# Kernel optimization log

Measured on AMD Instinct MI355X. Metric: run time of the kernel, lower is better.

The kernel has to match this reference:

```python
import jax, jax.numpy as jnp
import numpy as np

# Vim-S config
B, L, D, DEPTH = 16, 197, 384, 24
DI, DS, DTR = 768, 16, 24  # d_inner=2*D, d_state, dt_rank=ceil(D/16)
NUM_CLASSES = 1000
EPS = 1e-5


def setup_inputs() -> dict:
    key = jax.random.key(0)
    ks = jax.random.split(key, 12)
    f = jnp.float32
    rn = lambda k, shp, s=0.02: jax.random.normal(k, shp, f) * s
    inp = {
        'x': jax.random.normal(ks[0], (B, 3, 224, 224), f),
        'patch_w': rn(ks[1], (D, 3, 16, 16)),
        'patch_b': jnp.zeros((D,), f),
        'cls_token': rn(ks[2], (1, 1, D)),
        'pos_embed': rn(ks[3], (1, L, D)),
        'in_proj_w': rn(ks[4], (DEPTH, 2 * DI, D)),
        'conv_w': rn(ks[5], (DEPTH, DI, 1, 4), 0.1),  # depthwise causal conv, d_conv=4
        'conv_b': jnp.zeros((DEPTH, DI), f),
        'x_proj_w': rn(ks[6], (DEPTH, DTR + 2 * DS, DI)),
        'dt_proj_w': rn(ks[7], (DEPTH, DI, DTR), 0.1),
        'dt_proj_b': jnp.full((DEPTH, DI), float(np.log(np.expm1(0.01))), f),
        'A_log': jnp.log(jnp.broadcast_to(jnp.arange(1, DS + 1, dtype=f), (DEPTH, DI, DS))),
        'D_ssm': jnp.ones((DEPTH, DI), f),
        'out_proj_w': rn(ks[8], (DEPTH, D, DI)),
        'norm_w': jnp.ones((DEPTH, D), f),
        'norm_b': jnp.zeros((DEPTH, D), f),
        'normf_w': jnp.ones((D,), f),
        'normf_b': jnp.zeros((D,), f),
        'head_w': rn(ks[9], (NUM_CLASSES, D)),
        'head_b': jnp.zeros((NUM_CLASSES,), f),
    }
    return inp


def _ln(u, w, b):
    mu = u.mean(-1, keepdims=True)
    v = ((u - mu) ** 2).mean(-1, keepdims=True)
    return (u - mu) * jax.lax.rsqrt(v + EPS) * w + b


def _silu(u):
    return u * jax.nn.sigmoid(u)


def _mixer(u, Win, Wc, bc, Wx, Wdt, bdt, Alog, Dp, Wout):
    # u: [B, L, D]
    xz = jnp.einsum('bld,ed->ble', u, Win)            # [B, L, 2*DI]
    xc, z = jnp.split(xz, 2, axis=-1)
    # causal depthwise conv1d (d_conv=4): pad 3 on the left
    xt = jnp.pad(xc.transpose(0, 2, 1), ((0, 0), (0, 0), (3, 0)))
    xt = jax.lax.conv_general_dilated(xt, Wc, (1,), 'VALID',
                                      dimension_numbers=('NCH', 'OIH', 'NCH'),
                                      feature_group_count=DI)
    xc = _silu((xt + bc[None, :, None]).transpose(0, 2, 1))  # [B, L, DI]
    dbl = jnp.einsum('bld,ed->ble', xc, Wx)           # [B, L, DTR+2*DS]
    dt = jax.nn.softplus(jnp.einsum('blr,dr->bld', dbl[..., :DTR], Wdt) + bdt)
    Bm = dbl[..., DTR:DTR + DS]                       # [B, L, DS]
    Cm = dbl[..., DTR + DS:]                          # [B, L, DS]
    A = -jnp.exp(Alog)                                # [DI, DS]
    dA = jnp.exp(jnp.einsum('bld,dn->bldn', dt, A))   # [B, L, DI, DS]
    dBx = jnp.einsum('bld,bln->bldn', dt * xc, Bm)    # [B, L, DI, DS]

    def step(h, inps):
        dA_t, dBx_t, C_t = inps
        h = dA_t * h + dBx_t                          # [B, DI, DS]
        return h, jnp.einsum('bdn,bn->bd', h, C_t)

    h0 = jnp.zeros((u.shape[0], DI, DS), u.dtype)
    _, ys = jax.lax.scan(step, h0, (dA.transpose(1, 0, 2, 3),
                                    dBx.transpose(1, 0, 2, 3),
                                    Cm.transpose(1, 0, 2)))
    y = ys.transpose(1, 0, 2) + xc * Dp               # [B, L, DI]
    y = y * _silu(z)
    return jnp.einsum('ble,de->bld', y, Wout)         # [B, L, D]


def reference(x, patch_w, patch_b, cls_token, pos_embed, in_proj_w, conv_w, conv_b,
              x_proj_w, dt_proj_w, dt_proj_b, A_log, D_ssm, out_proj_w,
              norm_w, norm_b, normf_w, normf_b, head_w, head_b):
    b = x.shape[0]
    # patch embed: Conv2d(3, D, 16, stride 16)
    feat = jax.lax.conv_general_dilated(x, patch_w, (16, 16), 'VALID',
                                        dimension_numbers=('NCHW', 'OIHW', 'NCHW'))
    feat = feat + patch_b[None, :, None, None]
    tokens = feat.reshape(b, D, -1).transpose(0, 2, 1)          # [B, 196, D]
    h = jnp.concatenate([jnp.broadcast_to(cls_token, (b, 1, D)), tokens], axis=1)
    h = h + pos_embed                                           # [B, 197, D]

    def layer(carry, p):
        hid, res = carry
        Win, Wc, bc, Wx, Wdt, bdt, Alog, Dp, Wout, nw, nb = p
        res = res + hid                # (hidden + residual), first layer: residual = hidden
        hid = _mixer(_ln(res, nw, nb), Win, Wc, bc, Wx, Wdt, bdt, Alog, Dp, Wout)
        return (hid, res), None

    (hid, res), _ = jax.lax.scan(layer, (h, jnp.zeros_like(h)),
                                 (in_proj_w, conv_w, conv_b, x_proj_w, dt_proj_w,
                                  dt_proj_b, A_log, D_ssm, out_proj_w, norm_w, norm_b))
    out = _ln(res + hid, normf_w, normf_b)
    return out[:, 0] @ head_w.T + head_b                        # [B, num_classes]
```

## Files before the change

kernel.cpp:

```cpp
#include <hip/hip_runtime.h>
#include <hip/hip_bf16.h>
#include <math.h>

#define BB     16
#define LL     197
#define DD     384
#define DEPTH  24
#define DI     768
#define DSN    16
#define DTR    24
#define NC     1000
#define TT     (BB*LL)
#define NPATCH 196
#define EPSV   1e-5f

#define NCHUNK 12
#define CH     17

typedef __attribute__((ext_vector_type(8))) short short8;
typedef __attribute__((ext_vector_type(4))) short short4v;
typedef __attribute__((ext_vector_type(4))) float f32x4;

__device__ __forceinline__ short f2bf(float f) {
  union { float f; unsigned u; } v; v.f = f;
  unsigned u = v.u + 0x7fffu + ((v.u >> 16) & 1u);
  return (short)(u >> 16);
}

__device__ __forceinline__ void gload16(const short* g, const short* l) {
  __builtin_amdgcn_global_load_lds(
      (const __attribute__((address_space(1))) unsigned int*)g,
      (__attribute__((address_space(3))) unsigned int*)l, 16, 0, 0);
}

__global__ __launch_bounds__(256) void k_cvt4(const float* __restrict__ s0, short* __restrict__ d0, int n0,
                                              const float* __restrict__ s1, short* __restrict__ d1, int n1,
                                              const float* __restrict__ s2, short* __restrict__ d2, int n2,
                                              const float* __restrict__ s3, short* __restrict__ d3, int n3,
                                              int b0, int b1, int b2) {
  int blk = blockIdx.x;
  const float* src; short* dst; int n; int lb;
  if (blk < b0)      { src = s0; dst = d0; n = n0; lb = blk; }
  else if (blk < b1) { src = s1; dst = d1; n = n1; lb = blk - b0; }
  else if (blk < b2) { src = s2; dst = d2; n = n2; lb = blk - b1; }
  else               { src = s3; dst = d3; n = n3; lb = blk - b2; }
  int i = (lb * 256 + threadIdx.x) * 4;
  if (i + 3 < n) {
    float4 v = *(const float4*)&src[i];
    short4v o = {f2bf(v.x), f2bf(v.y), f2bf(v.z), f2bf(v.w)};
    *(short4v*)&dst[i] = o;
  } else {
    for (int j = 0; i + j < n && j < 4; j++) dst[i + j] = f2bf(src[i + j]);
  }
}

__global__ __launch_bounds__(256) void k_init(const float* __restrict__ cls,
                                              const float* __restrict__ pos,
                                              float* __restrict__ res) {
  int i = blockIdx.x * 256 + threadIdx.x;
  if (i < BB * DD) {
    int b = i / DD, d = i % DD;
    res[(size_t)(b * LL) * DD + d] = cls[d] + pos[d];
  }
}

__global__ __launch_bounds__(256) void k_patch(const float* __restrict__ x,
                                               const float* __restrict__ pw,
                                               const float* __restrict__ pb,
                                               const float* __restrict__ pos,
                                               float* __restrict__ res) {
  __shared__ short sA[64 * 40];
  __shared__ short sB[64 * 40];
  const int tid = threadIdx.x;
  const int m0 = blockIdx.x * 64, n0 = blockIdx.y * 64;
  const int srow = tid >> 2;
  const int skq = (tid & 3) * 8;
  const int lane = tid & 63, w = tid >> 6;
  const int wm = (w >> 1) * 32, wn = (w & 1) * 32;
  const int fr = lane & 15;
  const int fk = (lane >> 4) * 8;
  f32x4 acc[2][2] = {};
  const int m = m0 + srow;
  const int b = m / NPATCH;
  const int p = m % NPATCH;
  const int ph = p / 14, pwi = p % 14;
  const float* Wrow = pw + (size_t)(n0 + srow) * 768 + skq;
  for (int k0 = 0; k0 < 768; k0 += 32) {
    int k = k0 + skq;
    int c = k >> 8, rr = (k >> 4) & 15, kw = k & 15;
    const float* xrow = &x[(size_t)(((b * 3 + c) * 224) + (ph * 16 + rr)) * 224 +
                           (pwi * 16 + kw)];
    float4 a0 = *(const float4*)&xrow[0];
    float4 a1 = *(const float4*)&xrow[4];
    float4 b0 = *(const float4*)&Wrow[k0];
    float4 b1 = *(const float4*)&Wrow[k0 + 4];
    short8 av = {f2bf(a0.x), f2bf(a0.y), f2bf(a0.z), f2bf(a0.w),
                 f2bf(a1.x), f2bf(a1.y), f2bf(a1.z), f2bf(a1.w)};
    short8 bv = {f2bf(b0.x), f2bf(b0.y), f2bf(b0.z), f2bf(b0.w),
                 f2bf(b1.x), f2bf(b1.y), f2bf(b1.z), f2bf(b1.w)};
    *(short8*)&sA[srow * 40 + skq] = av;
    *(short8*)&sB[srow * 40 + skq] = bv;
    __syncthreads();
    short8 af0 = *(const short8*)&sA[(wm + fr) * 40 + fk];
    short8 af1 = *(const short8*)&sA[(wm + 16 + fr) * 40 + fk];
    short8 bf0 = *(const short8*)&sB[(wn + fr) * 40 + fk];
    short8 bf1 = *(const short8*)&sB[(wn + 16 + fr) * 40 + fk];
    acc[0][0] = __builtin_amdgcn_mfma_f32_16x16x32_bf16(af0, bf0, acc[0][0], 0, 0, 0);
    acc[0][1] = __builtin_amdgcn_mfma_f32_16x16x32_bf16(af0, bf1, acc[0][1], 0, 0, 0);
    acc[1][0] = __builtin_amdgcn_mfma_f32_16x16x32_bf16(af1, bf0, acc[1][0], 0, 0, 0);
    acc[1][1] = __builtin_amdgcn_mfma_f32_16x16x32_bf16(af1, bf1, acc[1][1], 0, 0, 0);
    __syncthreads();
  }
#pragma unroll
  for (int i = 0; i < 2; i++)
#pragma unroll
    for (int j = 0; j < 2; j++)
#pragma unroll
      for (int q = 0; q < 4; q++) {
        int mm = m0 + wm + i * 16 + (lane >> 4) * 4 + q;
        int nn = n0 + wn + j * 16 + (lane & 15);
        int b2 = mm / NPATCH, pp = mm % NPATCH;
        int tok = b2 * LL + 1 + pp;
        res[(size_t)tok * DD + nn] = acc[i][j][q] + pb[nn] + pos[(size_t)(1 + pp) * DD + nn];
      }
}

__global__ __launch_bounds__(256) void k_gemm128(const short* __restrict__ A, int lda,
                                                 const short* __restrict__ W, int ldb,
                                                 float* __restrict__ C, int ldc,
                                                 int M, int N, int K) {
  __shared__ short sA[128 * 32];
  __shared__ short sB[128 * 32];
  const int tid = threadIdx.x;
  const int lane = tid & 63, w = tid >> 6;
  const int m0 = blockIdx.x * 128, n0 = blockIdx.y * 128;
  const int wm = (w >> 1) * 64, wn = (w & 1) * 64;
  const int fr = lane & 15;
  const int fk = (lane >> 4) * 8;
  const int q0 = w * 2, q1 = w * 2 + 1;
  const int sr0 = q0 * 16 + (lane >> 2);
  const int sr1 = q1 * 16 + (lane >> 2);
  const int scol = (lane & 3) * 8;
  f32x4 acc[4][4] = {};
  const short* Ab0 = A + (size_t)(m0 + sr0) * lda + scol;
  const short* Ab1 = A + (size_t)(m0 + sr1) * lda + scol;
  const short* Bb0 = W + (size_t)(n0 + sr0) * ldb + scol;
  const short* Bb1 = W + (size_t)(n0 + sr1) * ldb + scol;
  for (int k0 = 0; k0 < K; k0 += 32) {
    gload16(Ab0 + k0, &sA[q0 * 512]);
    gload16(Ab1 + k0, &sA[q1 * 512]);
    gload16(Bb0 + k0, &sB[q0 * 512]);
    gload16(Bb1 + k0, &sB[q1 * 512]);
    __syncthreads();
    short8 af[4], bf[4];
#pragma unroll
    for (int i = 0; i < 4; i++) {
      af[i] = *(const short8*)&sA[(wm + i * 16 + fr) * 32 + fk];
      bf[i] = *(const short8*)&sB[(wn + i * 16 + fr) * 32 + fk];
    }
#pragma unroll
    for (int i = 0; i < 4; i++)
#pragma unroll
      for (int j = 0; j < 4; j++)
        acc[i][j] = __builtin_amdgcn_mfma_f32_16x16x32_bf16(af[i], bf[j], acc[i][j], 0, 0, 0);
    __syncthreads();
  }
#pragma unroll
  for (int i = 0; i < 4; i++)
#pragma unroll
    for (int j = 0; j < 4; j++)
#pragma unroll
      for (int q = 0; q < 4; q++) {
        int mm = m0 + wm + i * 16 + (lane >> 4) * 4 + q;
        int nn = n0 + wn + j * 16 + fr;
        if (mm < M) C[(size_t)mm * ldc + nn] = acc[i][j][q];
      }
}

__global__ __launch_bounds__(256) void k_gemm64(const short* __restrict__ A, int lda,
                                                const short* __restrict__ W, int ldb,
                                                float* __restrict__ C, int ldc,
                                                int M, int N, int K) {
  __shared__ short sA[64 * 32];
  __shared__ short sB[64 * 32];
  const int tid = threadIdx.x;
  const int lane = tid & 63, w = tid >> 6;
  const int m0 = blockIdx.x * 64, n0 = blockIdx.y * 64;
  const int wm = (w >> 1) * 32, wn = (w & 1) * 32;
  const int fr = lane & 15;
  const int fk = (lane >> 4) * 8;
  const int srow = w * 16 + (lane >> 2);
  const int scol = (lane & 3) * 8;
  f32x4 acc[2][2] = {};
  const short* Ab = A + (size_t)(m0 + srow) * lda + scol;
  const short* Bb = W + (size_t)(n0 + srow) * ldb + scol;
  for (int k0 = 0; k0 < K; k0 += 32) {
    gload16(Ab + k0, &sA[w * 512]);
    gload16(Bb + k0, &sB[w * 512]);
    __syncthreads();
    short8 af0 = *(const short8*)&sA[(wm + fr) * 32 + fk];
    short8 af1 = *(const short8*)&sA[(wm + 16 + fr) * 32 + fk];
    short8 bf0 = *(const short8*)&sB[(wn + fr) * 32 + fk];
    short8 bf1 = *(const short8*)&sB[(wn + 16 + fr) * 32 + fk];
    acc[0][0] = __builtin_amdgcn_mfma_f32_16x16x32_bf16(af0, bf0, acc[0][0], 0, 0, 0);
    acc[0][1] = __builtin_amdgcn_mfma_f32_16x16x32_bf16(af0, bf1, acc[0][1], 0, 0, 0);
    acc[1][0] = __builtin_amdgcn_mfma_f32_16x16x32_bf16(af1, bf0, acc[1][0], 0, 0, 0);
    acc[1][1] = __builtin_amdgcn_mfma_f32_16x16x32_bf16(af1, bf1, acc[1][1], 0, 0, 0);
    __syncthreads();
  }
#pragma unroll
  for (int i = 0; i < 2; i++)
#pragma unroll
    for (int j = 0; j < 2; j++)
#pragma unroll
      for (int q = 0; q < 4; q++) {
        int mm = m0 + wm + i * 16 + (lane >> 4) * 4 + q;
        int nn = n0 + wn + j * 16 + fr;
        if (mm < M) C[(size_t)mm * ldc + nn] += acc[i][j][q];
      }
}

__global__ __launch_bounds__(256) void k_conv(const float* __restrict__ xz,
                                              const float* __restrict__ wc,
                                              const float* __restrict__ bc,
                                              float* __restrict__ xc,
                                              short* __restrict__ xcbf) {
  int i = blockIdx.x * 256 + threadIdx.x;
  if (i >= TT * (DI / 4)) return;
  int eg = i % (DI / 4);
  int t = i / (DI / 4);
  int e = eg * 4;
  int b = t / LL, l = t % LL;
  const float* base = xz + (size_t)(b * LL) * (2 * DI) + e;
  float4 w0 = *(const float4*)&wc[(e + 0) * 4];
  float4 w1 = *(const float4*)&wc[(e + 1) * 4];
  float4 w2 = *(const float4*)&wc[(e + 2) * 4];
  float4 w3 = *(const float4*)&wc[(e + 3) * 4];
  float4 acc = *(const float4*)&bc[e];
  if (l >= 3) {
    float4 xv = *(const float4*)&base[(size_t)(l - 3) * (2 * DI)];
    acc.x += xv.x * w0.x; acc.y += xv.y * w1.x; acc.z += xv.z * w2.x; acc.w += xv.w * w3.x;
  }
  if (l >= 2) {
    float4 xv = *(const float4*)&base[(size_t)(l - 2) * (2 * DI)];
    acc.x += xv.x * w0.y; acc.y += xv.y * w1.y; acc.z += xv.z * w2.y; acc.w += xv.w * w3.y;
  }
  if (l >= 1) {
    float4 xv = *(const float4*)&base[(size_t)(l - 1) * (2 * DI)];
    acc.x += xv.x * w0.z; acc.y += xv.y * w1.z; acc.z += xv.z * w2.z; acc.w += xv.w * w3.z;
  }
  {
    float4 xv = *(const float4*)&base[(size_t)l * (2 * DI)];
    acc.x += xv.x * w0.w; acc.y += xv.y * w1.w; acc.z += xv.z * w2.w; acc.w += xv.w * w3.w;
  }
  acc.x = acc.x / (1.f + __expf(-acc.x));
  acc.y = acc.y / (1.f + __expf(-acc.y));
  acc.z = acc.z / (1.f + __expf(-acc.z));
  acc.w = acc.w / (1.f + __expf(-acc.w));
  *(float4*)&xc[(size_t)t * DI + e] = acc;
  short4v ov = {f2bf(acc.x), f2bf(acc.y), f2bf(acc.z), f2bf(acc.w)};
  *(short4v*)&xcbf[(size_t)t * DI + e] = ov;
}

__global__ __launch_bounds__(256, 1) void k_xd(const short* __restrict__ xcbf,
                                               const short* __restrict__ wx,
                                               const short* __restrict__ wdt,
                                               const float* __restrict__ dbias,
                                               float* __restrict__ dbl,
                                               float* __restrict__ dtb) {
  __shared__ short sDT[16 * 40];
  const int tid = threadIdx.x;
  const int t0 = blockIdx.x * 16;
  const int lane = tid & 63, w = tid >> 6;
  const int fr = lane & 15;
  const int fk = (lane >> 4) * 8;
  f32x4 acc0 = {}, acc1 = {};
  const short* Arow = xcbf + (size_t)(t0 + fr) * DI + fk;
  const short* Wrow = wx + (size_t)(w * 16 + fr) * DI + fk;
#pragma unroll
  for (int k0 = 0; k0 < DI; k0 += 64) {
    short8 af0 = *(const short8*)&Arow[k0];
    short8 bf0 = *(const short8*)&Wrow[k0];
    short8 af1 = *(const short8*)&Arow[k0 + 32];
    short8 bf1 = *(const short8*)&Wrow[k0 + 32];
    acc0 = __builtin_amdgcn_mfma_f32_16x16x32_bf16(af0, bf0, acc0, 0, 0, 0);
    acc1 = __builtin_amdgcn_mfma_f32_16x16x32_bf16(af1, bf1, acc1, 0, 0, 0);
  }
  f32x4 accx = acc0 + acc1;
  {
    int nn = w * 16 + fr;
#pragma unroll
    for (int q = 0; q < 4; q++) {
      int row = (lane >> 4) * 4 + q;
      int t = t0 + row;
      if (nn >= DTR && nn < 56) dbl[(size_t)t * 56 + nn] = accx[q];
      if (w < 2) sDT[row * 40 + nn] = (nn < DTR) ? f2bf(accx[q]) : (short)0;
    }
  }
  __syncthreads();
  short8 adt = *(const short8*)&sDT[fr * 40 + fk];
  const int g = lane >> 4;
#pragma unroll
  for (int jj = 0; jj < 12; jj++) {
    int j = w * 12 + jj;
    short8 bdt = short8{0, 0, 0, 0, 0, 0, 0, 0};
    if (g < 3) bdt = *(const short8*)&wdt[(size_t)(j * 16 + fr) * DTR + g * 8];
    f32x4 p = {};
    p = __builtin_amdgcn_mfma_f32_16x16x32_bf16(adt, bdt, p, 0, 0, 0);
    int nc = j * 16 + fr;
    float bv = dbias[nc];
#pragma unroll
    for (int q = 0; q < 4; q++) {
      int t = t0 + (lane >> 4) * 4 + q;
      float v = p[q] + bv;
      v = (v > 20.f) ? v : __logf(1.f + __expf(v));
      dtb[(size_t)t * DI + nc] = v;
    }
  }
}

__global__ __launch_bounds__(256) void k_scan1(const float* __restrict__ dt,
                                               const float* __restrict__ xc,
                                               const float* __restrict__ dbl,
                                               const float* __restrict__ Alog,
                                               float* __restrict__ Aprod,
                                               float* __restrict__ Hend) {
  const int tid = threadIdx.x;
  const int e = blockIdx.x * 128 + (tid >> 1);
  const int nh = tid & 1;
  const int b = blockIdx.y;
  const int c = blockIdx.z;
  float4 al0 = *(const float4*)&Alog[(size_t)e * DSN + nh * 8];
  float4 al1 = *(const float4*)&Alog[(size_t)e * DSN + nh * 8 + 4];
  float negA[8] = {-__expf(al0.x), -__expf(al0.y), -__expf(al0.z), -__expf(al0.w),
                   -__expf(al1.x), -__expf(al1.y), -__expf(al1.z), -__expf(al1.w)};
  float h[8] = {};
  float asum = 0.f;
  const int l0 = c * CH;
  const int l1 = (l0 + CH < LL) ? (l0 + CH) : LL;
  const size_t tbase = (size_t)b * LL;
  for (int l = l0; l < l1; l++) {
    size_t t = tbase + l;
    float dtv = dt[t * DI + e];
    float xcv = xc[t * DI + e];
    float4 B0 = *(const float4*)&dbl[t * 56 + DTR + nh * 8];
    float4 B1 = *(const float4*)&dbl[t * 56 + DTR + nh * 8 + 4];
    float dx = dtv * xcv;
    float Bv[8] = {B0.x, B0.y, B0.z, B0.w, B1.x, B1.y, B1.z, B1.w};
#pragma unroll
    for (int j = 0; j < 8; j++)
      h[j] = __expf(dtv * negA[j]) * h[j] + dx * Bv[j];
    asum += dtv;
  }
  size_t ci = (((size_t)c * BB + b) * DI + e) * DSN + nh * 8;
  *(float4*)&Aprod[ci] = float4{__expf(asum * negA[0]), __expf(asum * negA[1]),
                                __expf(asum * negA[2]), __expf(asum * negA[3])};
  *(float4*)&Aprod[ci + 4] = float4{__expf(asum * negA[4]), __expf(asum * negA[5]),
                                    __expf(asum * negA[6]), __expf(asum * negA[7])};
  *(float4*)&Hend[ci] = float4{h[0], h[1], h[2], h[3]};
  *(float4*)&Hend[ci + 4] = float4{h[4], h[5], h[6], h[7]};
}

__global__ __launch_bounds__(256) void k_scan2(const float* __restrict__ dt,
                                               const float* __restrict__ xc,
                                               const float* __restrict__ xz,
                                               const float* __restrict__ dbl,
                                               const float* __restrict__ Alog,
                                               const float* __restrict__ Dp,
                                               const float* __restrict__ Aprod,
                                               const float* __restrict__ Hend,
                                               short* __restrict__ ybf) {
  const int tid = threadIdx.x;
  const int e = blockIdx.x * 128 + (tid >> 1);
  const int nh = tid & 1;
  const int b = blockIdx.y;
  const int c = blockIdx.z;
  float4 al0 = *(const float4*)&Alog[(size_t)e * DSN + nh * 8];
  float4 al1 = *(const float4*)&Alog[(size_t)e * DSN + nh * 8 + 4];
  float negA[8] = {-__expf(al0.x), -__expf(al0.y), -__expf(al0.z), -__expf(al0.w),
                   -__expf(al1.x), -__expf(al1.y), -__expf(al1.z), -__expf(al1.w)};
  const float dpv = Dp[e];
  float h[8] = {};
  const size_t cstride = (size_t)BB * DI * DSN;
  const size_t cbase = (((size_t)b * DI + e) * DSN) + nh * 8;
  for (int cp = 0; cp < c; cp++) {
    size_t ci = (size_t)cp * cstride + cbase;
    float4 a0 = *(const float4*)&Aprod[ci];
    float4 a1 = *(const float4*)&Aprod[ci + 4];
    float4 e0 = *(const float4*)&Hend[ci];
    float4 e1 = *(const float4*)&Hend[ci + 4];
    h[0] = a0.x * h[0] + e0.x; h[1] = a0.y * h[1] + e0.y;
    h[2] = a0.z * h[2] + e0.z; h[3] = a0.w * h[3] + e0.w;
    h[4] = a1.x * h[4] + e1.x; h[5] = a1.y * h[5] + e1.y;
    h[6] = a1.z * h[6] + e1.z; h[7] = a1.w * h[7] + e1.w;
  }
  const int l0 = c * CH;
  const int l1 = (l0 + CH < LL) ? (l0 + CH) : LL;
  const size_t tbase = (size_t)b * LL;
  for (int l = l0; l < l1; l++) {
    size_t t = tbase + l;
    float dtv = dt[t * DI + e];
    float xcv = xc[t * DI + e];
    float zv = xz[t * (2 * DI) + DI + e];
    float4 B0 = *(const float4*)&dbl[t * 56 + DTR + nh * 8];
    float4 B1 = *(const float4*)&dbl[t * 56 + DTR + nh * 8 + 4];
    float4 C0 = *(const float4*)&dbl[t * 56 + DTR + DSN + nh * 8];
    float4 C1 = *(const float4*)&dbl[t * 56 + DTR + DSN + nh * 8 + 4];
    float dx = dtv * xcv;
    float Bv[8] = {B0.x, B0.y, B0.z, B0.w, B1.x, B1.y, B1.z, B1.w};
    float Cv[8] = {C0.x, C0.y, C0.z, C0.w, C1.x, C1.y, C1.z, C1.w};
    float acc = 0.f;
#pragma unroll
    for (int j = 0; j < 8; j++) {
      h[j] = __expf(dtv * negA[j]) * h[j] + dx * Bv[j];
      acc += h[j] * Cv[j];
    }
    acc += __shfl_xor(acc, 1);
    if (nh == 0) {
      float sz = zv * (1.f / (1.f + __expf(-zv)));
      ybf[t * DI + e] = f2bf((acc + xcv * dpv) * sz);
    }
  }
}

__global__ __launch_bounds__(256) void k_ln(const float* __restrict__ res,
                                            short* __restrict__ u,
                                            const float* __restrict__ nw,
                                            const float* __restrict__ nb) {
  const int lane = threadIdx.x & 63;
  const int t = blockIdx.x * 4 + (threadIdx.x >> 6);
  float r[6];
  float s = 0.f, sq = 0.f;
#pragma unroll
  for (int j = 0; j < 6; j++) {
    int d = lane + j * 64;
    float v = res[(size_t)t * DD + d];
    r[j] = v;
    s += v; sq += v * v;
  }
#pragma unroll
  for (int o = 32; o > 0; o >>= 1) { s += __shfl_xor(s, o); sq += __shfl_xor(sq, o); }
  float mu = s * (1.f / 384.f);
  float var = sq * (1.f / 384.f) - mu * mu;
  float rs = rsqrtf(var + EPSV);
#pragma unroll
  for (int j = 0; j < 6; j++) {
    int d = lane + j * 64;
    u[(size_t)t * DD + d] = f2bf((r[j] - mu) * rs * nw[d] + nb[d]);
  }
}

__global__ __launch_bounds__(256) void k_final(const float* __restrict__ res,
                                               const float* __restrict__ nfw,
                                               const float* __restrict__ nfb,
                                               const float* __restrict__ hw,
                                               const float* __restrict__ hb,
                                               float* __restrict__ out) {
  const int b = blockIdx.y;
  const int c0 = blockIdx.x * 125;
  const int tid = threadIdx.x;
  __shared__ float u0[DD];
  __shared__ float ls[4], lq[4];
  const size_t t0 = (size_t)b * LL * DD;
  float v0 = res[t0 + tid];
  float v1 = (tid < 128) ? res[t0 + 256 + tid] : 0.f;
  float s = v0 + v1, sq = v0 * v0 + v1 * v1;
#pragma unroll
  for (int o = 32; o > 0; o >>= 1) { s += __shfl_xor(s, o); sq += __shfl_xor(sq, o); }
  if ((tid & 63) == 0) { ls[tid >> 6] = s; lq[tid >> 6] = sq; }
  __syncthreads();
  float st = ls[0] + ls[1] + ls[2] + ls[3];
  float qt = lq[0] + lq[1] + lq[2] + lq[3];
  float mu = st * (1.f / 384.f);
  float var = qt * (1.f / 384.f) - mu * mu;
  float rs = rsqrtf(var + EPSV);
  u0[tid] = (v0 - mu) * rs * nfw[tid] + nfb[tid];
  if (tid < 128) u0[256 + tid] = (v1 - mu) * rs * nfw[256 + tid] + nfb[256 + tid];
  __syncthreads();
  int c = c0 + tid;
  if (tid < 125 && c < NC) {
    float acc = hb[c];
    const float* wrow = hw + (size_t)c * DD;
    for (int d = 0; d < DD; d += 4) {
      float4 w4 = *(const float4*)&wrow[d];
      acc += u0[d] * w4.x + u0[d + 1] * w4.y + u0[d + 2] * w4.z + u0[d + 3] * w4.w;
    }
    out[(size_t)b * NC + c] = acc;
  }
}

extern "C" void kernel_launch(void* const* d_in, const int* in_sizes, int n_in,
                              void* d_out, int out_size, void* d_ws, size_t ws_size,
                              hipStream_t stream) {
  const float* x       = (const float*)d_in[0];
  const float* patch_w = (const float*)d_in[1];
  const float* patch_b = (const float*)d_in[2];
  const float* cls     = (const float*)d_in[3];
  const float* pos     = (const float*)d_in[4];
  const float* in_proj = (const float*)d_in[5];
  const float* conv_w  = (const float*)d_in[6];
  const float* conv_b  = (const float*)d_in[7];
  const float* x_proj  = (const float*)d_in[8];
  const float* dt_w    = (const float*)d_in[9];
  const float* dt_b    = (const float*)d_in[10];
  const float* A_log   = (const float*)d_in[11];
  const float* D_ssm   = (const float*)d_in[12];
  const float* out_w   = (const float*)d_in[13];
  const float* norm_w  = (const float*)d_in[14];
  const float* norm_b  = (const float*)d_in[15];
  const float* normf_w = (const float*)d_in[16];
  const float* normf_b = (const float*)d_in[17];
  const float* head_w  = (const float*)d_in[18];
  const float* head_b  = (const float*)d_in[19];
  float* out = (float*)d_out;

  float* ws = (float*)d_ws;
  float* res = ws;  ws += (size_t)TT * DD;
  float* u_r = ws;  ws += (size_t)TT * DD;
  float* xzb = ws;  ws += (size_t)TT * 2 * DI;
  float* xcb = ws;  ws += (size_t)TT * DI;
  float* dbl = ws;  ws += (size_t)TT * 56;
  float* dtb = ws;  ws += (size_t)TT * DI;
  float* ybf_r = ws; ws += (size_t)TT * DI / 2;
  float* xcbf_r = ws; ws += (size_t)TT * DI / 2;
  float* Aprod = ws; ws += (size_t)NCHUNK * BB * DI * DSN;
  float* Hend  = ws; ws += (size_t)NCHUNK * BB * DI * DSN;
  short* winbf  = (short*)ws; ws += (size_t)DEPTH * 2 * DI * DD / 2;
  short* woutbf = (short*)ws; ws += (size_t)DEPTH * DD * DI / 2;
  short* wxbf   = (short*)ws; ws += (size_t)DEPTH * 56 * DI / 2;
  short* wdtbf  = (short*)ws; ws += (size_t)DEPTH * DI * DTR / 2;

  short* u    = (short*)u_r;
  short* ybf  = (short*)ybf_r;
  short* xcbf = (short*)xcbf_r;

  {
    int n1 = DEPTH * 2 * DI * DD;
    int n2 = DEPTH * DD * DI;
    int n3 = DEPTH * 56 * DI;
    int n4 = DEPTH * DI * DTR;
    int g1 = (n1 / 4 + 255) / 256;
    int g2 = (n2 / 4 + 255) / 256;
    int g3 = (n3 / 4 + 255) / 256;
    int g4 = (n4 / 4 + 255) / 256;
    k_cvt4<<<g1 + g2 + g3 + g4, 256, 0, stream>>>(
        in_proj, winbf, n1, out_w, woutbf, n2, x_proj, wxbf, n3, dt_w, wdtbf, n4,
        g1, g1 + g2, g1 + g2 + g3);
  }

  k_init<<<(BB * DD + 255) / 256, 256, 0, stream>>>(cls, pos, res);
  k_patch<<<dim3(49, 6), 256, 0, stream>>>(x, patch_w, patch_b, pos, res);

  for (int layer = 0; layer < DEPTH; layer++) {
    k_ln<<<TT / 4, 256, 0, stream>>>(res, u, norm_w + layer * DD,
                                     norm_b + layer * DD);
    k_gemm128<<<dim3(25, 12), 256, 0, stream>>>(
        u, DD, winbf + (size_t)layer * 2 * DI * DD, DD, xzb, 2 * DI, TT, 2 * DI, DD);
    k_conv<<<(TT * (DI / 4) + 255) / 256, 256, 0, stream>>>(
        xzb, conv_w + layer * DI * 4, conv_b + layer * DI, xcb, xcbf);
    k_xd<<<dim3(TT / 16), 256, 0, stream>>>(
        xcbf, wxbf + (size_t)layer * 56 * DI, wdtbf + (size_t)layer * DI * DTR,
        dt_b + layer * DI, dbl, dtb);
    k_scan1<<<dim3(DI / 128, BB, NCHUNK - 1), 256, 0, stream>>>(
        dtb, xcb, dbl, A_log + (size_t)layer * DI * DSN, Aprod, Hend);
    k_scan2<<<dim3(DI / 128, BB, NCHUNK), 256, 0, stream>>>(
        dtb, xcb, xzb, dbl, A_log + (size_t)layer * DI * DSN,
        D_ssm + layer * DI, Aprod, Hend, ybf);
    k_gemm64<<<dim3(50, 6), 256, 0, stream>>>(
        ybf, DI, woutbf + (size_t)layer * DD * DI, DI, res, DD, TT, DD, DI);
  }

  k_final<<<dim3(8, BB), 256, 0, stream>>>(res, normf_w, normf_b, head_w, head_b, out);
}
```

Before: 2.632 ms.

## Fuse two-pass chunked selective scan into one kernel with LDS carry exchange

```diff
diff --git a/kernel.cpp b/kernel.cpp
--- a/kernel.cpp
+++ b/kernel.cpp
@@ -319,84 +319,57 @@
   }
 }
 
-__global__ __launch_bounds__(256) void k_scan1(const float* __restrict__ dt,
-                                               const float* __restrict__ xc,
-                                               const float* __restrict__ dbl,
-                                               const float* __restrict__ Alog,
-                                               float* __restrict__ Aprod,
-                                               float* __restrict__ Hend) {
+__global__ __launch_bounds__(768) void k_scan(const float* __restrict__ dt,
+                                              const float* __restrict__ xc,
+                                              const float* __restrict__ xz,
+                                              const float* __restrict__ dbl,
+                                              const float* __restrict__ Alog,
+                                              const float* __restrict__ Dp,
+                                              short* __restrict__ ybf) {
+  __shared__ float carry[NCHUNK][32][2][17];
   const int tid = threadIdx.x;
-  const int e = blockIdx.x * 128 + (tid >> 1);
-  const int nh = tid & 1;
-  const int b = blockIdx.y;
-  const int c = blockIdx.z;
+  const int c  = tid >> 6;
+  const int nh = (tid >> 5) & 1;
+  const int el = tid & 31;
+  const int e  = blockIdx.x * 32 + el;
+  const int b  = blockIdx.y;
   float4 al0 = *(const float4*)&Alog[(size_t)e * DSN + nh * 8];
   float4 al1 = *(const float4*)&Alog[(size_t)e * DSN + nh * 8 + 4];
   float negA[8] = {-__expf(al0.x), -__expf(al0.y), -__expf(al0.z), -__expf(al0.w),
                    -__expf(al1.x), -__expf(al1.y), -__expf(al1.z), -__expf(al1.w)};
-  float h[8] = {};
-  float asum = 0.f;
   const int l0 = c * CH;
   const int l1 = (l0 + CH < LL) ? (l0 + CH) : LL;
   const size_t tbase = (size_t)b * LL;
-  for (int l = l0; l < l1; l++) {
-    size_t t = tbase + l;
-    float dtv = dt[t * DI + e];
-    float xcv = xc[t * DI + e];
-    float4 B0 = *(const float4*)&dbl[t * 56 + DTR + nh * 8];
-    float4 B1 = *(const float4*)&dbl[t * 56 + DTR + nh * 8 + 4];
-    float dx = dtv * xcv;
-    float Bv[8] = {B0.x, B0.y, B0.z, B0.w, B1.x, B1.y, B1.z, B1.w};
+  if (c < NCHUNK - 1) {
+    float h[8] = {};
+    float asum = 0.f;
+    for (int l = l0; l < l1; l++) {
+      size_t t = tbase + l;
+      float dtv = dt[t * DI + e];
+      float xcv = xc[t * DI + e];
+      float4 B0 = *(const float4*)&dbl[t * 56 + DTR + nh * 8];
+      float4 B1 = *(const float4*)&dbl[t * 56 + DTR + nh * 8 + 4];
+      float dx = dtv * xcv;
+      float Bv[8] = {B0.x, B0.y, B0.z, B0.w, B1.x, B1.y, B1.z, B1.w};
+#pragma unroll
+      for (int j = 0; j < 8; j++)
+        h[j] = __expf(dtv * negA[j]) * h[j] + dx * Bv[j];
+      asum += dtv;
+    }
+#pragma unroll
+    for (int j = 0; j < 8; j++) {
+      carry[c][el][nh][j]     = __expf(asum * negA[j]);
+      carry[c][el][nh][8 + j] = h[j];
+    }
+  }
+  __syncthreads();
+  float h[8] = {};
+  for (int cp = 0; cp < c; cp++) {
 #pragma unroll
     for (int j = 0; j < 8; j++)
-      h[j] = __expf(dtv * negA[j]) * h[j] + dx * Bv[j];
-    asum += dtv;
-  }
-  size_t ci = (((size_t)c * BB + b) * DI + e) * DSN + nh * 8;
-  *(float4*)&Aprod[ci] = float4{__expf(asum * negA[0]), __expf(asum * negA[1]),
-                                __expf(asum * negA[2]), __expf(asum * negA[3])};
-  *(float4*)&Aprod[ci + 4] = float4{__expf(asum * negA[4]), __expf(asum * negA[5]),
-                                    __expf(asum * negA[6]), __expf(asum * negA[7])};
-  *(float4*)&Hend[ci] = float4{h[0], h[1], h[2], h[3]};
-  *(float4*)&Hend[ci + 4] = float4{h[4], h[5], h[6], h[7]};
-}
-
-__global__ __launch_bounds__(256) void k_scan2(const float* __restrict__ dt,
-                                               const float* __restrict__ xc,
-                                               const float* __restrict__ xz,
-                                               const float* __restrict__ dbl,
-                                               const float* __restrict__ Alog,
-                                               const float* __restrict__ Dp,
-                                               const float* __restrict__ Aprod,
-                                               const float* __restrict__ Hend,
-                                               short* __restrict__ ybf) {
-  const int tid = threadIdx.x;
-  const int e = blockIdx.x * 128 + (tid >> 1);
-  const int nh = tid & 1;
-  const int b = blockIdx.y;
-  const int c = blockIdx.z;
-  float4 al0 = *(const float4*)&Alog[(size_t)e * DSN + nh * 8];
-  float4 al1 = *(const float4*)&Alog[(size_t)e * DSN + nh * 8 + 4];
-  float negA[8] = {-__expf(al0.x), -__expf(al0.y), -__expf(al0.z), -__expf(al0.w),
-                   -__expf(al1.x), -__expf(al1.y), -__expf(al1.z), -__expf(al1.w)};
+      h[j] = carry[cp][el][nh][j] * h[j] + carry[cp][el][nh][8 + j];
+  }
   const float dpv = Dp[e];
-  float h[8] = {};
-  const size_t cstride = (size_t)BB * DI * DSN;
-  const size_t cbase = (((size_t)b * DI + e) * DSN) + nh * 8;
-  for (int cp = 0; cp < c; cp++) {
-    size_t ci = (size_t)cp * cstride + cbase;
-    float4 a0 = *(const float4*)&Aprod[ci];
-    float4 a1 = *(const float4*)&Aprod[ci + 4];
-    float4 e0 = *(const float4*)&Hend[ci];
-    float4 e1 = *(const float4*)&Hend[ci + 4];
-    h[0] = a0.x * h[0] + e0.x; h[1] = a0.y * h[1] + e0.y;
-    h[2] = a0.z * h[2] + e0.z; h[3] = a0.w * h[3] + e0.w;
-    h[4] = a1.x * h[4] + e1.x; h[5] = a1.y * h[5] + e1.y;
-    h[6] = a1.z * h[6] + e1.z; h[7] = a1.w * h[7] + e1.w;
-  }
-  const int l0 = c * CH;
-  const int l1 = (l0 + CH < LL) ? (l0 + CH) : LL;
-  const size_t tbase = (size_t)b * LL;
   for (int l = l0; l < l1; l++) {
     size_t t = tbase + l;
     float dtv = dt[t * DI + e];
@@ -415,7 +388,7 @@
       h[j] = __expf(dtv * negA[j]) * h[j] + dx * Bv[j];
       acc += h[j] * Cv[j];
     }
-    acc += __shfl_xor(acc, 1);
+    acc += __shfl_xor(acc, 32);
     if (nh == 0) {
       float sz = zv * (1.f / (1.f + __expf(-zv)));
       ybf[t * DI + e] = f2bf((acc + xcv * dpv) * sz);
@@ -523,8 +496,6 @@
   float* dtb = ws;  ws += (size_t)TT * DI;
   float* ybf_r = ws; ws += (size_t)TT * DI / 2;
   float* xcbf_r = ws; ws += (size_t)TT * DI / 2;
-  float* Aprod = ws; ws += (size_t)NCHUNK * BB * DI * DSN;
-  float* Hend  = ws; ws += (size_t)NCHUNK * BB * DI * DSN;
   short* winbf  = (short*)ws; ws += (size_t)DEPTH * 2 * DI * DD / 2;
   short* woutbf = (short*)ws; ws += (size_t)DEPTH * DD * DI / 2;
   short* wxbf   = (short*)ws; ws += (size_t)DEPTH * 56 * DI / 2;
@@ -561,11 +532,9 @@
     k_xd<<<dim3(TT / 16), 256, 0, stream>>>(
         xcbf, wxbf + (size_t)layer * 56 * DI, wdtbf + (size_t)layer * DI * DTR,
         dt_b + layer * DI, dbl, dtb);
-    k_scan1<<<dim3(DI / 128, BB, NCHUNK - 1), 256, 0, stream>>>(
-        dtb, xcb, dbl, A_log + (size_t)layer * DI * DSN, Aprod, Hend);
-    k_scan2<<<dim3(DI / 128, BB, NCHUNK), 256, 0, stream>>>(
+    k_scan<<<dim3(DI / 32, BB), 768, 0, stream>>>(
         dtb, xcb, xzb, dbl, A_log + (size_t)layer * DI * DSN,
-        D_ssm + layer * DI, Aprod, Hend, ybf);
+        D_ssm + layer * DI, ybf);
     k_gemm64<<<dim3(50, 6), 256, 0, stream>>>(
         ybf, DI, woutbf + (size_t)layer * DD * DI, DI, res, DD, TT, DD, DI);
   }
```

Result: faster. 2.480 ms (-5.8%).
